# Performance work log

Measured on AMD Instinct MI355X. Metric: run time of the kernel, lower is better.

## Reference

```python
import jax, jax.numpy as jnp
import numpy as np

B, C, S = 16, 256, 1024
P_TOT, L = 24, 64
HEADS, DH = 8, 64
INNER = HEADS * DH
SPLITS = 8
SCALE = DH ** -0.5


def setup_inputs() -> dict:
    key = jax.random.key(0)
    k0, k1, k2, k3, k4 = jax.random.split(key, 5)
    w_scale = C ** -0.5  # Linear default-ish init scale, keeps softmax sane
    return {
        "x": jax.random.normal(k0, (B, C, S), jnp.float32),
        "prototypes": jax.random.normal(k1, (P_TOT, C, L), jnp.float32),
        "Wq": jax.random.normal(k2, (3, C, INNER), jnp.float32) * w_scale,
        "Wk": jax.random.normal(k3, (3, C, INNER), jnp.float32) * w_scale,
        "Wv": jax.random.normal(k4, (3, C, INNER), jnp.float32) * w_scale,
    }


def reference(x, prototypes, Wq, Wk, Wv):
    # x: [B, C, S] -> [B, S, C]; prototypes: [24, C, L]
    xp = jnp.transpose(x, (0, 2, 1))
    dists, idxs = [], []
    for i in range(3):  # fixed small loop over the 3 projection groups
        pg = prototypes[i * SPLITS:(i + 1) * SPLITS]          # [P, C, L]
        pp = jnp.transpose(pg, (0, 2, 1))                     # [P, L, C]
        # Q is identical across batch (the torch .repeat is a broadcast):
        q = (pp @ Wq[i]).reshape(SPLITS, L, HEADS, DH)        # [P, L, H, Dh]
        k = (xp @ Wk[i]).reshape(B, S, HEADS, DH)             # [B, S, H, Dh]
        v = (xp @ Wv[i]).reshape(B, S, HEADS, DH)
        dots = jnp.einsum('plhd,bshd->bhpls', q, k) * SCALE   # [B, H, P, L, S]
        attn = jax.nn.softmax(dots, axis=-1)
        out = jnp.einsum('bhpls,bshd->bhpld', attn, v)        # [B, H, P, L, Dh]
        out = jnp.transpose(out, (0, 2, 3, 1, 4)).reshape(B, SPLITS, L, INNER)
        q_full = q.reshape(SPLITS, L, INNER)[None]            # broadcast over B
        dist = jnp.mean((q_full - out) ** 2, axis=(2, 3))     # [B, P]
        heat = attn.mean(axis=(1, 3))                         # [B, P, S]
        dists.append(dist)
        idxs.append(jnp.argmax(heat, axis=-1))                # [B, P]
    return jnp.concatenate(dists, axis=1), jnp.concatenate(idxs, axis=1)
```

## Files before the change

kernel.cpp:

```cpp
#include <hip/hip_runtime.h>
#include <hip/hip_bf16.h>

#define Bq 16
#define Cc 256
#define Ss 1024
#define Ll 64
#define Hh 8
#define DHd 64
#define INN 512
#define Pp 8
#define KSC 0.18033688011111772f

#define QSLOT    262144
#define MDSLOT   131072
#define HEATSLOT 1048576
#define OUTSLOT  8388608
#define KSLOT    8388608
#define WSLOT    393216
#define HALFO    4194304

typedef short s16x8 __attribute__((ext_vector_type(8)));
typedef float f32x4 __attribute__((ext_vector_type(4)));
typedef unsigned u32x2 __attribute__((ext_vector_type(2)));
typedef unsigned u32x4 __attribute__((ext_vector_type(4)));

__device__ __forceinline__ unsigned short f2bf(float f) {
    unsigned u = __builtin_bit_cast(unsigned, f);
    u += 0x7FFF + ((u >> 16) & 1);
    return (unsigned short)(u >> 16);
}
__device__ __forceinline__ float bf2f(unsigned short h) {
    return __builtin_bit_cast(float, (unsigned)h << 16);
}
__device__ __forceinline__ unsigned cvt_pk_bf16(float a, float b) {
    unsigned r;
    asm volatile("v_cvt_pk_bf16_f32 %0, %1, %2" : "=v"(r) : "v"(a), "v"(b));
    return r;
}
__device__ __forceinline__ u32x2 ds_tr16(const unsigned short* p) {
    u32x2 d;
    asm volatile("ds_read_b64_tr_b16 %0, %1"
                 : "=v"(d)
                 : "v"((const __attribute__((address_space(3))) unsigned short*)p)
                 : "memory");
    return d;
}

__global__ __launch_bounds__(256) void wsplit_kernel(
        const float* __restrict__ Wk, const float* __restrict__ Wv,
        unsigned short* __restrict__ Wth, unsigned short* __restrict__ Wtl,
        unsigned short* __restrict__ Wvh) {
    __shared__ float tile[64][65];
    int blk = blockIdx.x;
    int i = blk >> 6, rem = blk & 63, mat = rem >> 5, ns = (rem >> 2) & 7, cb = rem & 3;
    int n0 = ns * 64, c0 = cb * 64, t = threadIdx.x;
    const float* W = (mat == 0 ? Wk : Wv) + (size_t)i * Cc * INN;
#pragma unroll
    for (int it = 0; it < 16; ++it) {
        int idx = t + it * 256; int cc = idx >> 6, nn = idx & 63;
        tile[cc][nn] = W[(size_t)(c0 + cc) * INN + n0 + nn];
    }
    __syncthreads();
#pragma unroll
    for (int it = 0; it < 16; ++it) {
        int idx = t + it * 256; int nn = idx >> 6, cc = idx & 63;
        float v = tile[cc][nn];
        unsigned short hi = f2bf(v);
        size_t o = (size_t)i * 131072 + (size_t)(n0 + nn) * Cc + c0 + cc;
        if (mat == 0) { Wth[o] = hi; Wtl[o] = f2bf(v - bf2f(hi)); }
        else          { Wvh[o] = hi; }
    }
}

__global__ __launch_bounds__(256) void qk_kernel(const float* __restrict__ prot,
                                                 const float* __restrict__ Wq,
                                                 float* __restrict__ qout) {
    __shared__ float pcol[4][256];
    int blk = blockIdx.x;
    int i = blk >> 7, rem = blk & 127, p = rem >> 4, l4 = rem & 15;
    int t = threadIdx.x;
    const float* W = Wq + (size_t)i * Cc * INN;
#pragma unroll
    for (int it = 0; it < 4; ++it) {
        int idx = t + it * 256; int ll = idx >> 8, cc = idx & 255;
        pcol[ll][cc] = prot[((size_t)(i * Pp + p) * Cc + cc) * Ll + l4 * 4 + ll];
    }
    __syncthreads();
    float a0[4] = {0, 0, 0, 0}, a1[4] = {0, 0, 0, 0};
#pragma unroll 4
    for (int c = 0; c < Cc; ++c) {
        float w0 = W[c * INN + t], w1 = W[c * INN + t + 256];
#pragma unroll
        for (int ll = 0; ll < 4; ++ll) {
            a0[ll] += pcol[ll][c] * w0;
            a1[ll] += pcol[ll][c] * w1;
        }
    }
#pragma unroll
    for (int ll = 0; ll < 4; ++ll) {
        float* qo = qout + (size_t)i * QSLOT + (size_t)(p * 64 + l4 * 4 + ll) * INN;
        qo[t] = a0[ll]; qo[t + 256] = a1[ll];
    }
}

__device__ __forceinline__ int xs_idx4(int s, int col4) {
    return s * 64 + (col4 ^ (s & 7));
}

__global__ __launch_bounds__(512, 2) void kv_kernel(
        const float* __restrict__ x, const unsigned short* __restrict__ WthA,
        const unsigned short* __restrict__ WtlA, const unsigned short* __restrict__ WvhA,
        unsigned short* __restrict__ Kh, unsigned short* __restrict__ Kl,
        unsigned short* __restrict__ Vt, int i0) {
    __shared__ unsigned xs[64 * 256];
    int bx = blockIdx.x & 255, i_local = blockIdx.x >> 8;
    int i = i0 + i_local;
    int b = bx >> 4, sb = bx & 15;
    int t = threadIdx.x, w = t >> 6, lane = t & 63, c = lane & 15, g = lane >> 4;
    int h = w;
    const unsigned short* wth = WthA + (size_t)i * 131072;
    const unsigned short* wtl = WtlA + (size_t)i * 131072;
    const unsigned short* wvh = WvhA + (size_t)i * 131072;
    unsigned short* Khp = Kh + (size_t)i_local * KSLOT;
    unsigned short* Klp = Kl + (size_t)i_local * KSLOT;
    unsigned short* Vtp = Vt + (size_t)i_local * KSLOT;

#pragma unroll
    for (int it = 0; it < 8; ++it) {
        int unit = t + it * 512;
        int ch = unit >> 4, sq = unit & 15;
        float4 v = *(const float4*)(x + ((size_t)b * Cc + ch) * Ss + sb * 64 + sq * 4);
        float vv[4] = {v.x, v.y, v.z, v.w};
#pragma unroll
        for (int e = 0; e < 4; ++e) {
            int s = sq * 4 + e;
            unsigned short hi = f2bf(vv[e]);
            unsigned short lo = f2bf(vv[e] - bf2f(hi));
            xs[s * 256 + ((ch >> 2) ^ (s & 7)) * 4 + (ch & 3)] =
                ((unsigned)hi << 16) | lo;
        }
    }
    __syncthreads();

    f32x4 accK[4][4], accV[4][4];
#pragma unroll
    for (int a = 0; a < 4; ++a)
#pragma unroll
      for (int s = 0; s < 4; ++s) {
        accK[a][s] = (f32x4){0.f, 0.f, 0.f, 0.f};
        accV[a][s] = (f32x4){0.f, 0.f, 0.f, 0.f};
      }

#pragma unroll
    for (int cs = 0; cs < 8; ++cs) {
        s16x8 xh[4], xl[4];
#pragma unroll
        for (int st = 0; st < 4; ++st) {
            int s = st * 16 + c;
            uint4 q0 = ((const uint4*)xs)[xs_idx4(s, cs * 8 + g * 2)];
            uint4 q1 = ((const uint4*)xs)[xs_idx4(s, cs * 8 + g * 2 + 1)];
            unsigned wrd[8] = {q0.x, q0.y, q0.z, q0.w, q1.x, q1.y, q1.z, q1.w};
            s16x8 fh, fl;
#pragma unroll
            for (int e = 0; e < 8; ++e) {
                fh[e] = (short)(wrd[e] >> 16);
                fl[e] = (short)(wrd[e] & 0xFFFF);
            }
            xh[st] = fh; xl[st] = fl;
        }
        int c0 = cs * 32 + g * 8;
#pragma unroll
        for (int nt = 0; nt < 4; ++nt) {
            int n = h * 64 + nt * 16 + c;
            s16x8 bh = __builtin_bit_cast(s16x8, *(const uint4*)(wth + (size_t)n * Cc + c0));
            s16x8 bl = __builtin_bit_cast(s16x8, *(const uint4*)(wtl + (size_t)n * Cc + c0));
            s16x8 bv = __builtin_bit_cast(s16x8, *(const uint4*)(wvh + (size_t)n * Cc + c0));
#pragma unroll
            for (int st = 0; st < 4; ++st) {
                accK[nt][st] = __builtin_amdgcn_mfma_f32_16x16x32_bf16(bh, xh[st], accK[nt][st], 0, 0, 0);
                accK[nt][st] = __builtin_amdgcn_mfma_f32_16x16x32_bf16(bh, xl[st], accK[nt][st], 0, 0, 0);
                accK[nt][st] = __builtin_amdgcn_mfma_f32_16x16x32_bf16(bl, xh[st], accK[nt][st], 0, 0, 0);
                accV[st][nt] = __builtin_amdgcn_mfma_f32_16x16x32_bf16(xh[st], bv, accV[st][nt], 0, 0, 0);
            }
        }
    }

#pragma unroll
    for (int nt = 0; nt < 4; ++nt)
#pragma unroll
      for (int st = 0; st < 4; ++st) {
        size_t kb = ((size_t)(b * Hh + h) * Ss + sb * 64 + st * 16 + c) * DHd
                    + nt * 16 + g * 4;
        unsigned short h0 = f2bf(accK[nt][st][0]), h1 = f2bf(accK[nt][st][1]);
        unsigned short h2 = f2bf(accK[nt][st][2]), h3 = f2bf(accK[nt][st][3]);
        uint2 ph; ph.x = h0 | ((unsigned)h1 << 16); ph.y = h2 | ((unsigned)h3 << 16);
        *(uint2*)(Khp + kb) = ph;
        unsigned short l0 = f2bf(accK[nt][st][0] - bf2f(h0));
        unsigned short l1 = f2bf(accK[nt][st][1] - bf2f(h1));
        unsigned short l2 = f2bf(accK[nt][st][2] - bf2f(h2));
        unsigned short l3 = f2bf(accK[nt][st][3] - bf2f(h3));
        uint2 pl; pl.x = l0 | ((unsigned)l1 << 16); pl.y = l2 | ((unsigned)l3 << 16);
        *(uint2*)(Klp + kb) = pl;
        size_t vb = ((size_t)(b * Hh + h) * DHd + nt * 16 + c) * Ss
                    + sb * 64 + st * 16 + g * 4;
        unsigned short v0 = f2bf(accV[st][nt][0]), v1 = f2bf(accV[st][nt][1]);
        unsigned short v2 = f2bf(accV[st][nt][2]), v3 = f2bf(accV[st][nt][3]);
        uint2 pv; pv.x = v0 | ((unsigned)v1 << 16); pv.y = v2 | ((unsigned)v3 << 16);
        *(uint2*)(Vtp + vb) = pv;
      }
}

__global__ __launch_bounds__(512, 2) void passA_kernel(
        const float* __restrict__ q, const unsigned short* __restrict__ Kh,
        float* __restrict__ md, int i0) {
    __shared__ unsigned short Klds[4096];
    int bx = blockIdx.x & 255, i_local = blockIdx.x >> 8;
    int i = i0 + i_local;
    int b = bx >> 4, h = (bx >> 1) & 7, sh = bx & 1;
    int t = threadIdx.x, p = t >> 6, lane = t & 63, c = lane & 15, g = lane >> 4;
    const float* qb = q + (size_t)i * QSLOT;
    const unsigned short* Khp = Kh + (size_t)i_local * KSLOT;

    s16x8 qh[4][2];
#pragma unroll
    for (int mt = 0; mt < 4; ++mt)
#pragma unroll
      for (int kt = 0; kt < 2; ++kt) {
        const float* qp = qb + (size_t)(p * 64 + mt * 16 + c) * INN + h * 64 + kt * 32 + g * 8;
        s16x8 f;
#pragma unroll
        for (int e = 0; e < 8; ++e) f[e] = (short)f2bf(qp[e] * KSC);
        qh[mt][kt] = f;
      }

    float d[4][4];
#pragma unroll
    for (int a = 0; a < 4; ++a)
#pragma unroll
      for (int r = 0; r < 4; ++r) d[a][r] = 0.f;

    int srow = t >> 3, g8 = t & 7, swz = g8 ^ (srow & 7);
    size_t rowb = (size_t)(b * Hh + h) * Ss;
    uint4 rK = *(const uint4*)(Khp + (rowb + sh * 512 + srow) * DHd + g8 * 8);

    for (int ch = 0; ch < 8; ++ch) {
        int sbase = sh * 512 + ch * 64;
        ((uint4*)Klds)[srow * 8 + swz] = rK;
        __syncthreads();
        if (ch < 7)
            rK = *(const uint4*)(Khp + (rowb + sbase + 64 + srow) * DHd + g8 * 8);

        f32x4 acc[4][4];
#pragma unroll
        for (int a = 0; a < 4; ++a)
#pragma unroll
          for (int s = 0; s < 4; ++s) acc[a][s] = (f32x4){0.f, 0.f, 0.f, 0.f};

#pragma unroll
        for (int kt = 0; kt < 2; ++kt)
#pragma unroll
          for (int st = 0; st < 4; ++st) {
            int srw = st * 16 + c;
            s16x8 kh = __builtin_bit_cast(s16x8,
                ((const uint4*)Klds)[srw * 8 + ((kt * 4 + g) ^ (srw & 7))]);
#pragma unroll
            for (int mt = 0; mt < 4; ++mt)
                acc[mt][st] = __builtin_amdgcn_mfma_f32_16x16x32_bf16(
                    qh[mt][kt], kh, acc[mt][st], 0, 0, 0);
          }

#pragma unroll
        for (int mt = 0; mt < 4; ++mt)
#pragma unroll
          for (int r = 0; r < 4; ++r)
            d[mt][r] += (__builtin_exp2f(acc[mt][0][r]) + __builtin_exp2f(acc[mt][1][r]))
                      + (__builtin_exp2f(acc[mt][2][r]) + __builtin_exp2f(acc[mt][3][r]));
        __syncthreads();
    }

    float* mdp = md + (size_t)i_local * MDSLOT;
#pragma unroll
    for (int mt = 0; mt < 4; ++mt)
#pragma unroll
      for (int r = 0; r < 4; ++r) {
        float v = d[mt][r];
        v += __shfl_xor(v, 1); v += __shfl_xor(v, 2);
        v += __shfl_xor(v, 4); v += __shfl_xor(v, 8);
        if (c == 0) {
            int row = mt * 16 + g * 4 + r;
            mdp[(((size_t)(b * Hh + h) * 2 + sh) * Pp + p) * Ll + row] = v;
        }
      }
}

__global__ __launch_bounds__(512) void passB_kernel(
        const float* __restrict__ q, const unsigned short* __restrict__ Kh,
        const unsigned short* __restrict__ Kl, const unsigned short* __restrict__ Vt,
        const float* __restrict__ md, float* __restrict__ heatp,
        unsigned short* __restrict__ outp, int i0) {
    __shared__ unsigned short Khl_[4096];
    __shared__ unsigned short Kll_[4096];
    __shared__ unsigned short Vtl_[4096];
    __shared__ unsigned short plds[8 * 2048];
    int bx = blockIdx.x & 255, i_local = blockIdx.x >> 8;
    int i = i0 + i_local;
    int b = bx >> 4, h = (bx >> 1) & 7, sh = bx & 1;
    int t = threadIdx.x, p = t >> 6, lane = t & 63, c = lane & 15, g = lane >> 4;
    const float* qb = q + (size_t)i * QSLOT;
    const unsigned short* Khp = Kh + (size_t)i_local * KSLOT;
    const unsigned short* Klp = Kl + (size_t)i_local * KSLOT;
    const unsigned short* Vtp = Vt + (size_t)i_local * KSLOT;
    const float* mdp = md + (size_t)i_local * MDSLOT;
    float* hpp = heatp + (size_t)i_local * HEATSLOT;
    unsigned short* opp = outp + (size_t)i_local * OUTSLOT;

    float rdf[4][4];
#pragma unroll
    for (int mt = 0; mt < 4; ++mt)
#pragma unroll
      for (int r = 0; r < 4; ++r) {
        int row = mt * 16 + g * 4 + r;
        size_t j0 = (((size_t)(b * Hh + h) * 2 + 0) * Pp + p) * Ll + row;
        size_t j1 = (((size_t)(b * Hh + h) * 2 + 1) * Pp + p) * Ll + row;
        rdf[mt][r] = 1.0f / (mdp[j0] + mdp[j1]);
      }

    s16x8 qh[4][2], ql[4][2];
#pragma unroll
    for (int mt = 0; mt < 4; ++mt)
#pragma unroll
      for (int kt = 0; kt < 2; ++kt) {
        const float* qp = qb + (size_t)(p * 64 + mt * 16 + c) * INN + h * 64 + kt * 32 + g * 8;
        s16x8 fh, fl;
#pragma unroll
        for (int e = 0; e < 8; ++e) {
            float v = qp[e] * KSC;
            unsigned short hi = f2bf(v);
            fh[e] = (short)hi;
            fl[e] = (short)f2bf(v - bf2f(hi));
        }
        qh[mt][kt] = fh; ql[mt][kt] = fl;
      }

    f32x4 o[4][4];
#pragma unroll
    for (int a = 0; a < 4; ++a)
#pragma unroll
      for (int s = 0; s < 4; ++s) o[a][s] = (f32x4){0.f, 0.f, 0.f, 0.f};

    int srow = t >> 3, g8 = t & 7, swz = g8 ^ (srow & 7);
    size_t rowK = (size_t)(b * Hh + h) * Ss;
    size_t rowV = ((size_t)(b * Hh + h) * DHd + srow) * Ss;
    uint4 rK = *(const uint4*)(Khp + (rowK + sh * 512 + srow) * DHd + g8 * 8);
    uint4 rL = *(const uint4*)(Klp + (rowK + sh * 512 + srow) * DHd + g8 * 8);
    uint4 rV = *(const uint4*)(Vtp + rowV + sh * 512 + g8 * 8);

    unsigned short* pwb = plds + p * 2048 + ((c >> 2) & 1) * 256 + (c & 3) * 16 + g * 4;
    const unsigned short* trb = plds + p * 2048 + g * 64 + c;

    for (int ch = 0; ch < 8; ++ch) {
        int sbase = sh * 512 + ch * 64;
        int dst = srow * 8 + swz;
        ((uint4*)Khl_)[dst] = rK;
        ((uint4*)Kll_)[dst] = rL;
        ((uint4*)Vtl_)[dst] = rV;
        __syncthreads();
        if (ch < 7) {
            rK = *(const uint4*)(Khp + (rowK + sbase + 64 + srow) * DHd + g8 * 8);
            rL = *(const uint4*)(Klp + (rowK + sbase + 64 + srow) * DHd + g8 * 8);
            rV = *(const uint4*)(Vtp + rowV + sbase + 64 + g8 * 8);
        }

#pragma unroll
        for (int half = 0; half < 2; ++half) {
            f32x4 sacc[4][2];
#pragma unroll
            for (int a = 0; a < 4; ++a)
#pragma unroll
              for (int s = 0; s < 2; ++s) sacc[a][s] = (f32x4){0.f, 0.f, 0.f, 0.f};

#pragma unroll
            for (int kt = 0; kt < 2; ++kt)
#pragma unroll
              for (int s2 = 0; s2 < 2; ++s2) {
                int srw = (half * 2 + s2) * 16 + c;
                int gi = srw * 8 + ((kt * 4 + g) ^ (srw & 7));
                s16x8 kh = __builtin_bit_cast(s16x8, ((const uint4*)Khl_)[gi]);
                s16x8 kl = __builtin_bit_cast(s16x8, ((const uint4*)Kll_)[gi]);
#pragma unroll
                for (int mt = 0; mt < 4; ++mt) {
                    sacc[mt][s2] = __builtin_amdgcn_mfma_f32_16x16x32_bf16(
                        qh[mt][kt], kh, sacc[mt][s2], 0, 0, 0);
                    sacc[mt][s2] = __builtin_amdgcn_mfma_f32_16x16x32_bf16(
                        qh[mt][kt], kl, sacc[mt][s2], 0, 0, 0);
                    sacc[mt][s2] = __builtin_amdgcn_mfma_f32_16x16x32_bf16(
                        ql[mt][kt], kh, sacc[mt][s2], 0, 0, 0);
                }
              }

#pragma unroll
            for (int s2 = 0; s2 < 2; ++s2) {
                float hs = 0.f;
#pragma unroll
                for (int mt = 0; mt < 4; ++mt) {
                    float pv0 = __builtin_exp2f(sacc[mt][s2][0]) * rdf[mt][0];
                    float pv1 = __builtin_exp2f(sacc[mt][s2][1]) * rdf[mt][1];
                    float pv2 = __builtin_exp2f(sacc[mt][s2][2]) * rdf[mt][2];
                    float pv3 = __builtin_exp2f(sacc[mt][s2][3]) * rdf[mt][3];
                    hs += (pv0 + pv1) + (pv2 + pv3);
                    uint2 pk;
                    pk.x = cvt_pk_bf16(pv0, pv1);
                    pk.y = cvt_pk_bf16(pv2, pv3);
                    *(uint2*)(pwb + mt * 512 + (s2 * 2 + (c >> 3)) * 64) = pk;
                }
                hs += __shfl_xor(hs, 16);
                hs += __shfl_xor(hs, 32);
                if (g == 0) {
                    int sgl = sbase + (half * 2 + s2) * 16 + c;
                    hpp[((size_t)(b * Pp + p) * Ss + sgl) * Hh + h] = hs;
                }
            }

            s16x8 vbf[4];
#pragma unroll
            for (int dht = 0; dht < 4; ++dht) {
                int row = dht * 16 + c;
                vbf[dht] = __builtin_bit_cast(s16x8,
                    ((const uint4*)Vtl_)[row * 8 + ((half * 4 + g) ^ (c & 7))]);
            }
            u32x2 ta[4][2];
#pragma unroll
            for (int mt = 0; mt < 4; ++mt) {
                ta[mt][0] = ds_tr16(trb + mt * 512);
                ta[mt][1] = ds_tr16(trb + mt * 512 + 256);
            }
            asm volatile("s_waitcnt lgkmcnt(0)" ::: "memory");
            __builtin_amdgcn_sched_barrier(0);
#pragma unroll
            for (int mt = 0; mt < 4; ++mt) {
                s16x8 pa = __builtin_bit_cast(s16x8,
                    (u32x4){ta[mt][0][0], ta[mt][0][1], ta[mt][1][0], ta[mt][1][1]});
#pragma unroll
                for (int dht = 0; dht < 4; ++dht)
                    o[mt][dht] = __builtin_amdgcn_mfma_f32_16x16x32_bf16(
                        pa, vbf[dht], o[mt][dht], 0, 0, 0);
            }
        }
        __syncthreads();
    }

#pragma unroll
    for (int mt = 0; mt < 4; ++mt)
#pragma unroll
      for (int dht = 0; dht < 4; ++dht)
#pragma unroll
        for (int r = 0; r < 4; ++r) {
            int row = mt * 16 + g * 4 + r;
            opp[(((((size_t)sh * Bq + b) * Hh + h) * Pp + p) * Ll + row) * DHd
                + dht * 16 + c] = f2bf(o[mt][dht][r]);
        }
}

__global__ __launch_bounds__(256) void fin_kernel(
        const float* __restrict__ heatp, const unsigned short* __restrict__ outp,
        const float* __restrict__ q, float* __restrict__ out, int i0) {
    __shared__ float rv[4];
    __shared__ int   ri[4];
    __shared__ float rs[4];
    int bx = blockIdx.x & 127, i_local = blockIdx.x >> 7;
    int i = i0 + i_local;
    int b = bx >> 3, p = bx & 7;
    int t = threadIdx.x, w = t >> 6, lane = t & 63;
    const float* qb = q + (size_t)i * QSLOT;
    const float* hp = heatp + (size_t)i_local * HEATSLOT;
    const unsigned short* ob = outp + (size_t)i_local * OUTSLOT;

    float best = -1e30f; int bidx = 0;
#pragma unroll
    for (int it = 0; it < 4; ++it) {
        int s = t + it * 256;
        const float* hv8 = hp + ((size_t)(b * Pp + p) * Ss + s) * Hh;
        float4 h0 = *(const float4*)hv8;
        float4 h1 = *(const float4*)(hv8 + 4);
        float hv = ((h0.x + h0.y) + (h0.z + h0.w)) + ((h1.x + h1.y) + (h1.z + h1.w));
        if (hv > best) { best = hv; bidx = s; }
    }
#pragma unroll
    for (int off = 1; off < 64; off <<= 1) {
        float vo = __shfl_xor(best, off);
        int   io = __shfl_xor(bidx, off);
        if (vo > best || (vo == best && io < bidx)) { best = vo; bidx = io; }
    }
    if (lane == 0) { rv[w] = best; ri[w] = bidx; }
    __syncthreads();
    if (t == 0) {
#pragma unroll
        for (int u = 1; u < 4; ++u)
            if (rv[u] > best || (rv[u] == best && ri[u] < bidx)) { best = rv[u]; bidx = ri[u]; }
        out[384 + b * 24 + i * Pp + p] = (float)bidx;
    }

    float sum = 0.f;
#pragma unroll 4
    for (int it = 0; it < 32; ++it) {
        int idx2 = t + it * 256;
        int dh4 = idx2 & 15, l = (idx2 >> 4) & 63, hh = idx2 >> 10;
        size_t base = ((size_t)((b * Hh + hh) * Pp + p) * 4096) + l * 64 + dh4 * 4;
        uint2 o0 = *(const uint2*)(ob + base);
        uint2 o1 = *(const uint2*)(ob + HALFO + base);
        float4 qv = *(const float4*)(qb + (size_t)(p * 64 + l) * INN + hh * 64 + dh4 * 4);
        float d0 = qv.x - (bf2f(o0.x & 0xFFFF) + bf2f(o1.x & 0xFFFF));
        float d1 = qv.y - (bf2f(o0.x >> 16)    + bf2f(o1.x >> 16));
        float d2 = qv.z - (bf2f(o0.y & 0xFFFF) + bf2f(o1.y & 0xFFFF));
        float d3 = qv.w - (bf2f(o0.y >> 16)    + bf2f(o1.y >> 16));
        sum += (d0 * d0 + d1 * d1) + (d2 * d2 + d3 * d3);
    }
#pragma unroll
    for (int off = 32; off; off >>= 1) sum += __shfl_down(sum, off);
    if (lane == 0) rs[w] = sum;
    __syncthreads();
    if (t == 0)
        out[b * 24 + i * Pp + p] = (rs[0] + rs[1] + rs[2] + rs[3]) / (float)(Ll * INN);
}

extern "C" void kernel_launch(void* const* d_in, const int* in_sizes, int n_in,
                              void* d_out, int out_size, void* d_ws, size_t ws_size,
                              hipStream_t stream) {
    const float* x    = (const float*)d_in[0];
    const float* prot = (const float*)d_in[1];
    const float* Wq   = (const float*)d_in[2];
    const float* Wk   = (const float*)d_in[3];
    const float* Wv   = (const float*)d_in[4];
    float* out = (float*)d_out;
    float* ws  = (float*)d_ws;

    const size_t needB = 220987392ull;
    bool batched = ws_size >= needB;
    size_t NS = batched ? 3 : 1;

    float* qbuf  = ws;
    float* md    = qbuf + 3 * QSLOT;
    float* heatp = md + NS * MDSLOT;
    unsigned short* outp = (unsigned short*)(heatp + NS * HEATSLOT);
    unsigned short* Kh  = outp + NS * OUTSLOT;
    unsigned short* Kl  = Kh + NS * KSLOT;
    unsigned short* Vt  = Kl + NS * KSLOT;
    unsigned short* Wth = Vt + NS * KSLOT;
    unsigned short* Wtl = Wth + 3 * WSLOT;
    unsigned short* Wvh = Wtl + 3 * WSLOT;

    wsplit_kernel<<<192, 256, 0, stream>>>(Wk, Wv, Wth, Wtl, Wvh);
    qk_kernel    <<<384, 256, 0, stream>>>(prot, Wq, qbuf);
    if (batched) {
        kv_kernel   <<<768, 512, 0, stream>>>(x, Wth, Wtl, Wvh, Kh, Kl, Vt, 0);
        passA_kernel<<<768, 512, 0, stream>>>(qbuf, Kh, md, 0);
        passB_kernel<<<768, 512, 0, stream>>>(qbuf, Kh, Kl, Vt, md, heatp, outp, 0);
        fin_kernel  <<<384, 256, 0, stream>>>(heatp, outp, qbuf, out, 0);
    } else {
        for (int i = 0; i < 3; ++i) {
            kv_kernel   <<<256, 512, 0, stream>>>(x, Wth, Wtl, Wvh, Kh, Kl, Vt, i);
            passA_kernel<<<256, 512, 0, stream>>>(qbuf, Kh, md, i);
            passB_kernel<<<256, 512, 0, stream>>>(qbuf, Kh, Kl, Vt, md, heatp, outp, i);
            fin_kernel  <<<128, 256, 0, stream>>>(heatp, outp, qbuf, out, i);
        }
    }
}
```

Before: 405.1 us.

## Switch split-bf16 compensated GEMMs to single fp16 MFMA passes

Replaces the hi/lo bf16 split (three MFMAs per product for K and scores) with a single fp16 MFMA per product. This drops the Kl buffer, Wtl weights and the ql/kl fragments, and halves the LDS footprint of x. It also folds the softmax normalizer into the score accumulator's initial value as -log2(denominator), removing a per-element multiply. This cuts MFMA work and memory traffic by roughly a factor of two to three in kv and passB, at the cost of fp16 range and precision risk on the scores, probabilities and outputs.

```diff
diff --git a/kernel.cpp b/kernel.cpp
--- a/kernel.cpp
+++ b/kernel.cpp
@@ -19,7 +19,8 @@
 #define WSLOT    393216
 #define HALFO    4194304
 
-typedef short s16x8 __attribute__((ext_vector_type(8)));
+typedef _Float16 f16x8 __attribute__((ext_vector_type(8)));
+typedef _Float16 f16x2 __attribute__((ext_vector_type(2)));
 typedef float f32x4 __attribute__((ext_vector_type(4)));
 typedef unsigned u32x2 __attribute__((ext_vector_type(2)));
 typedef unsigned u32x4 __attribute__((ext_vector_type(4)));
@@ -32,10 +33,9 @@
 __device__ __forceinline__ float bf2f(unsigned short h) {
     return __builtin_bit_cast(float, (unsigned)h << 16);
 }
-__device__ __forceinline__ unsigned cvt_pk_bf16(float a, float b) {
-    unsigned r;
-    asm volatile("v_cvt_pk_bf16_f32 %0, %1, %2" : "=v"(r) : "v"(a), "v"(b));
-    return r;
+__device__ __forceinline__ unsigned short f2h(float f) {
+    _Float16 h = (_Float16)f;
+    return __builtin_bit_cast(unsigned short, h);
 }
 __device__ __forceinline__ u32x2 ds_tr16(const unsigned short* p) {
     u32x2 d;
@@ -48,8 +48,7 @@
 
 __global__ __launch_bounds__(256) void wsplit_kernel(
         const float* __restrict__ Wk, const float* __restrict__ Wv,
-        unsigned short* __restrict__ Wth, unsigned short* __restrict__ Wtl,
-        unsigned short* __restrict__ Wvh) {
+        unsigned short* __restrict__ Wth, unsigned short* __restrict__ Wvh) {
     __shared__ float tile[64][65];
     int blk = blockIdx.x;
     int i = blk >> 6, rem = blk & 63, mat = rem >> 5, ns = (rem >> 2) & 7, cb = rem & 3;
@@ -65,10 +64,9 @@
     for (int it = 0; it < 16; ++it) {
         int idx = t + it * 256; int nn = idx >> 6, cc = idx & 63;
         float v = tile[cc][nn];
-        unsigned short hi = f2bf(v);
         size_t o = (size_t)i * 131072 + (size_t)(n0 + nn) * Cc + c0 + cc;
-        if (mat == 0) { Wth[o] = hi; Wtl[o] = f2bf(v - bf2f(hi)); }
-        else          { Wvh[o] = hi; }
+        if (mat == 0) Wth[o] = f2h(v);
+        else          Wvh[o] = f2h(v);
     }
 }
 
@@ -103,42 +101,32 @@
     }
 }
 
-__device__ __forceinline__ int xs_idx4(int s, int col4) {
-    return s * 64 + (col4 ^ (s & 7));
-}
-
 __global__ __launch_bounds__(512, 2) void kv_kernel(
         const float* __restrict__ x, const unsigned short* __restrict__ WthA,
-        const unsigned short* __restrict__ WtlA, const unsigned short* __restrict__ WvhA,
-        unsigned short* __restrict__ Kh, unsigned short* __restrict__ Kl,
-        unsigned short* __restrict__ Vt, int i0) {
-    __shared__ unsigned xs[64 * 256];
+        const unsigned short* __restrict__ WvhA,
+        unsigned short* __restrict__ Kh, unsigned short* __restrict__ Vt, int i0) {
+    __shared__ unsigned short xs[64 * 256];
     int bx = blockIdx.x & 255, i_local = blockIdx.x >> 8;
     int i = i0 + i_local;
     int b = bx >> 4, sb = bx & 15;
     int t = threadIdx.x, w = t >> 6, lane = t & 63, c = lane & 15, g = lane >> 4;
     int h = w;
     const unsigned short* wth = WthA + (size_t)i * 131072;
-    const unsigned short* wtl = WtlA + (size_t)i * 131072;
     const unsigned short* wvh = WvhA + (size_t)i * 131072;
     unsigned short* Khp = Kh + (size_t)i_local * KSLOT;
-    unsigned short* Klp = Kl + (size_t)i_local * KSLOT;
     unsigned short* Vtp = Vt + (size_t)i_local * KSLOT;
 
 #pragma unroll
     for (int it = 0; it < 8; ++it) {
         int unit = t + it * 512;
-        int ch = unit >> 4, sq = unit & 15;
-        float4 v = *(const float4*)(x + ((size_t)b * Cc + ch) * Ss + sb * 64 + sq * 4);
-        float vv[4] = {v.x, v.y, v.z, v.w};
-#pragma unroll
-        for (int e = 0; e < 4; ++e) {
-            int s = sq * 4 + e;
-            unsigned short hi = f2bf(vv[e]);
-            unsigned short lo = f2bf(vv[e] - bf2f(hi));
-            xs[s * 256 + ((ch >> 2) ^ (s & 7)) * 4 + (ch & 3)] =
-                ((unsigned)hi << 16) | lo;
-        }
+        int s = unit & 63, ch0 = (unit >> 6) * 4;
+        const float* xp = x + ((size_t)b * Cc + ch0) * Ss + sb * 64 + s;
+        float v0 = xp[0], v1 = xp[Ss], v2 = xp[2 * Ss], v3 = xp[3 * Ss];
+        uint2 pk;
+        pk.x = f2h(v0) | ((unsigned)f2h(v1) << 16);
+        pk.y = f2h(v2) | ((unsigned)f2h(v3) << 16);
+        int addr16 = s * 256 + (((ch0 >> 3) ^ (s & 7)) << 3) + (ch0 & 7);
+        *(uint2*)(xs + addr16) = pk;
     }
     __syncthreads();
 
@@ -153,34 +141,23 @@
 
 #pragma unroll
     for (int cs = 0; cs < 8; ++cs) {
-        s16x8 xh[4], xl[4];
+        f16x8 xf[4];
 #pragma unroll
         for (int st = 0; st < 4; ++st) {
             int s = st * 16 + c;
-            uint4 q0 = ((const uint4*)xs)[xs_idx4(s, cs * 8 + g * 2)];
-            uint4 q1 = ((const uint4*)xs)[xs_idx4(s, cs * 8 + g * 2 + 1)];
-            unsigned wrd[8] = {q0.x, q0.y, q0.z, q0.w, q1.x, q1.y, q1.z, q1.w};
-            s16x8 fh, fl;
-#pragma unroll
-            for (int e = 0; e < 8; ++e) {
-                fh[e] = (short)(wrd[e] >> 16);
-                fl[e] = (short)(wrd[e] & 0xFFFF);
-            }
-            xh[st] = fh; xl[st] = fl;
+            xf[st] = __builtin_bit_cast(f16x8,
+                ((const uint4*)xs)[s * 32 + ((cs * 4 + g) ^ (s & 7))]);
         }
         int c0 = cs * 32 + g * 8;
 #pragma unroll
         for (int nt = 0; nt < 4; ++nt) {
             int n = h * 64 + nt * 16 + c;
-            s16x8 bh = __builtin_bit_cast(s16x8, *(const uint4*)(wth + (size_t)n * Cc + c0));
-            s16x8 bl = __builtin_bit_cast(s16x8, *(const uint4*)(wtl + (size_t)n * Cc + c0));
-            s16x8 bv = __builtin_bit_cast(s16x8, *(const uint4*)(wvh + (size_t)n * Cc + c0));
+            f16x8 bk = __builtin_bit_cast(f16x8, *(const uint4*)(wth + (size_t)n * Cc + c0));
+            f16x8 bv = __builtin_bit_cast(f16x8, *(const uint4*)(wvh + (size_t)n * Cc + c0));
 #pragma unroll
             for (int st = 0; st < 4; ++st) {
-                accK[nt][st] = __builtin_amdgcn_mfma_f32_16x16x32_bf16(bh, xh[st], accK[nt][st], 0, 0, 0);
-                accK[nt][st] = __builtin_amdgcn_mfma_f32_16x16x32_bf16(bh, xl[st], accK[nt][st], 0, 0, 0);
-                accK[nt][st] = __builtin_amdgcn_mfma_f32_16x16x32_bf16(bl, xh[st], accK[nt][st], 0, 0, 0);
-                accV[st][nt] = __builtin_amdgcn_mfma_f32_16x16x32_bf16(xh[st], bv, accV[st][nt], 0, 0, 0);
+                accK[nt][st] = __builtin_amdgcn_mfma_f32_16x16x32_f16(bk, xf[st], accK[nt][st], 0, 0, 0);
+                accV[st][nt] = __builtin_amdgcn_mfma_f32_16x16x32_f16(xf[st], bv, accV[st][nt], 0, 0, 0);
             }
         }
     }
@@ -191,21 +168,15 @@
       for (int st = 0; st < 4; ++st) {
         size_t kb = ((size_t)(b * Hh + h) * Ss + sb * 64 + st * 16 + c) * DHd
                     + nt * 16 + g * 4;
-        unsigned short h0 = f2bf(accK[nt][st][0]), h1 = f2bf(accK[nt][st][1]);
-        unsigned short h2 = f2bf(accK[nt][st][2]), h3 = f2bf(accK[nt][st][3]);
-        uint2 ph; ph.x = h0 | ((unsigned)h1 << 16); ph.y = h2 | ((unsigned)h3 << 16);
+        uint2 ph;
+        ph.x = f2h(accK[nt][st][0]) | ((unsigned)f2h(accK[nt][st][1]) << 16);
+        ph.y = f2h(accK[nt][st][2]) | ((unsigned)f2h(accK[nt][st][3]) << 16);
         *(uint2*)(Khp + kb) = ph;
-        unsigned short l0 = f2bf(accK[nt][st][0] - bf2f(h0));
-        unsigned short l1 = f2bf(accK[nt][st][1] - bf2f(h1));
-        unsigned short l2 = f2bf(accK[nt][st][2] - bf2f(h2));
-        unsigned short l3 = f2bf(accK[nt][st][3] - bf2f(h3));
-        uint2 pl; pl.x = l0 | ((unsigned)l1 << 16); pl.y = l2 | ((unsigned)l3 << 16);
-        *(uint2*)(Klp + kb) = pl;
         size_t vb = ((size_t)(b * Hh + h) * DHd + nt * 16 + c) * Ss
                     + sb * 64 + st * 16 + g * 4;
-        unsigned short v0 = f2bf(accV[st][nt][0]), v1 = f2bf(accV[st][nt][1]);
-        unsigned short v2 = f2bf(accV[st][nt][2]), v3 = f2bf(accV[st][nt][3]);
-        uint2 pv; pv.x = v0 | ((unsigned)v1 << 16); pv.y = v2 | ((unsigned)v3 << 16);
+        uint2 pv;
+        pv.x = f2h(accV[st][nt][0]) | ((unsigned)f2h(accV[st][nt][1]) << 16);
+        pv.y = f2h(accV[st][nt][2]) | ((unsigned)f2h(accV[st][nt][3]) << 16);
         *(uint2*)(Vtp + vb) = pv;
       }
 }
@@ -221,16 +192,16 @@
     const float* qb = q + (size_t)i * QSLOT;
     const unsigned short* Khp = Kh + (size_t)i_local * KSLOT;
 
-    s16x8 qh[4][2];
+    f16x8 qf[4][2];
 #pragma unroll
     for (int mt = 0; mt < 4; ++mt)
 #pragma unroll
       for (int kt = 0; kt < 2; ++kt) {
         const float* qp = qb + (size_t)(p * 64 + mt * 16 + c) * INN + h * 64 + kt * 32 + g * 8;
-        s16x8 f;
-#pragma unroll
-        for (int e = 0; e < 8; ++e) f[e] = (short)f2bf(qp[e] * KSC);
-        qh[mt][kt] = f;
+        f16x8 f;
+#pragma unroll
+        for (int e = 0; e < 8; ++e) f[e] = (_Float16)(qp[e] * KSC);
+        qf[mt][kt] = f;
       }
 
     float d[4][4];
@@ -261,12 +232,12 @@
 #pragma unroll
           for (int st = 0; st < 4; ++st) {
             int srw = st * 16 + c;
-            s16x8 kh = __builtin_bit_cast(s16x8,
+            f16x8 kf = __builtin_bit_cast(f16x8,
                 ((const uint4*)Klds)[srw * 8 + ((kt * 4 + g) ^ (srw & 7))]);
 #pragma unroll
             for (int mt = 0; mt < 4; ++mt)
-                acc[mt][st] = __builtin_amdgcn_mfma_f32_16x16x32_bf16(
-                    qh[mt][kt], kh, acc[mt][st], 0, 0, 0);
+                acc[mt][st] = __builtin_amdgcn_mfma_f32_16x16x32_f16(
+                    qf[mt][kt], kf, acc[mt][st], 0, 0, 0);
           }
 
 #pragma unroll
@@ -295,11 +266,10 @@
 
 __global__ __launch_bounds__(512) void passB_kernel(
         const float* __restrict__ q, const unsigned short* __restrict__ Kh,
-        const unsigned short* __restrict__ Kl, const unsigned short* __restrict__ Vt,
+        const unsigned short* __restrict__ Vt,
         const float* __restrict__ md, float* __restrict__ heatp,
         unsigned short* __restrict__ outp, int i0) {
     __shared__ unsigned short Khl_[4096];
-    __shared__ unsigned short Kll_[4096];
     __shared__ unsigned short Vtl_[4096];
     __shared__ unsigned short plds[8 * 2048];
     int bx = blockIdx.x & 255, i_local = blockIdx.x >> 8;
@@ -308,13 +278,12 @@
     int t = threadIdx.x, p = t >> 6, lane = t & 63, c = lane & 15, g = lane >> 4;
     const float* qb = q + (size_t)i * QSLOT;
     const unsigned short* Khp = Kh + (size_t)i_local * KSLOT;
-    const unsigned short* Klp = Kl + (size_t)i_local * KSLOT;
     const unsigned short* Vtp = Vt + (size_t)i_local * KSLOT;
     const float* mdp = md + (size_t)i_local * MDSLOT;
     float* hpp = heatp + (size_t)i_local * HEATSLOT;
     unsigned short* opp = outp + (size_t)i_local * OUTSLOT;
 
-    float rdf[4][4];
+    f32x4 lgd[4];
 #pragma unroll
     for (int mt = 0; mt < 4; ++mt)
 #pragma unroll
@@ -322,24 +291,19 @@
         int row = mt * 16 + g * 4 + r;
         size_t j0 = (((size_t)(b * Hh + h) * 2 + 0) * Pp + p) * Ll + row;
         size_t j1 = (((size_t)(b * Hh + h) * 2 + 1) * Pp + p) * Ll + row;
-        rdf[mt][r] = 1.0f / (mdp[j0] + mdp[j1]);
+        lgd[mt][r] = -__builtin_log2f(mdp[j0] + mdp[j1]);
       }
 
-    s16x8 qh[4][2], ql[4][2];
+    f16x8 qf[4][2];
 #pragma unroll
     for (int mt = 0; mt < 4; ++mt)
 #pragma unroll
       for (int kt = 0; kt < 2; ++kt) {
         const float* qp = qb + (size_t)(p * 64 + mt * 16 + c) * INN + h * 64 + kt * 32 + g * 8;
-        s16x8 fh, fl;
-#pragma unroll
-        for (int e = 0; e < 8; ++e) {
-            float v = qp[e] * KSC;
-            unsigned short hi = f2bf(v);
-            fh[e] = (short)hi;
-            fl[e] = (short)f2bf(v - bf2f(hi));
-        }
-        qh[mt][kt] = fh; ql[mt][kt] = fl;
+        f16x8 f;
+#pragma unroll
+        for (int e = 0; e < 8; ++e) f[e] = (_Float16)(qp[e] * KSC);
+        qf[mt][kt] = f;
       }
 
     f32x4 o[4][4];
@@ -352,7 +316,6 @@
     size_t rowK = (size_t)(b * Hh + h) * Ss;
     size_t rowV = ((size_t)(b * Hh + h) * DHd + srow) * Ss;
     uint4 rK = *(const uint4*)(Khp + (rowK + sh * 512 + srow) * DHd + g8 * 8);
-    uint4 rL = *(const uint4*)(Klp + (rowK + sh * 512 + srow) * DHd + g8 * 8);
     uint4 rV = *(const uint4*)(Vtp + rowV + sh * 512 + g8 * 8);
 
     unsigned short* pwb = plds + p * 2048 + ((c >> 2) & 1) * 256 + (c & 3) * 16 + g * 4;
@@ -362,12 +325,10 @@
         int sbase = sh * 512 + ch * 64;
         int dst = srow * 8 + swz;
         ((uint4*)Khl_)[dst] = rK;
-        ((uint4*)Kll_)[dst] = rL;
         ((uint4*)Vtl_)[dst] = rV;
         __syncthreads();
         if (ch < 7) {
             rK = *(const uint4*)(Khp + (rowK + sbase + 64 + srow) * DHd + g8 * 8);
-            rL = *(const uint4*)(Klp + (rowK + sbase + 64 + srow) * DHd + g8 * 8);
             rV = *(const uint4*)(Vtp + rowV + sbase + 64 + g8 * 8);
         }
 
@@ -377,25 +338,19 @@
 #pragma unroll
             for (int a = 0; a < 4; ++a)
 #pragma unroll
-              for (int s = 0; s < 2; ++s) sacc[a][s] = (f32x4){0.f, 0.f, 0.f, 0.f};
+              for (int s = 0; s < 2; ++s) sacc[a][s] = lgd[a];
 
 #pragma unroll
             for (int kt = 0; kt < 2; ++kt)
 #pragma unroll
               for (int s2 = 0; s2 < 2; ++s2) {
                 int srw = (half * 2 + s2) * 16 + c;
-                int gi = srw * 8 + ((kt * 4 + g) ^ (srw & 7));
-                s16x8 kh = __builtin_bit_cast(s16x8, ((const uint4*)Khl_)[gi]);
-                s16x8 kl = __builtin_bit_cast(s16x8, ((const uint4*)Kll_)[gi]);
-#pragma unroll
-                for (int mt = 0; mt < 4; ++mt) {
-                    sacc[mt][s2] = __builtin_amdgcn_mfma_f32_16x16x32_bf16(
-                        qh[mt][kt], kh, sacc[mt][s2], 0, 0, 0);
-                    sacc[mt][s2] = __builtin_amdgcn_mfma_f32_16x16x32_bf16(
-                        qh[mt][kt], kl, sacc[mt][s2], 0, 0, 0);
-                    sacc[mt][s2] = __builtin_amdgcn_mfma_f32_16x16x32_bf16(
-                        ql[mt][kt], kh, sacc[mt][s2], 0, 0, 0);
-                }
+                f16x8 kf = __builtin_bit_cast(f16x8,
+                    ((const uint4*)Khl_)[srw * 8 + ((kt * 4 + g) ^ (srw & 7))]);
+#pragma unroll
+                for (int mt = 0; mt < 4; ++mt)
+                    sacc[mt][s2] = __builtin_amdgcn_mfma_f32_16x16x32_f16(
+                        qf[mt][kt], kf, sacc[mt][s2], 0, 0, 0);
               }
 
 #pragma unroll
@@ -403,14 +358,14 @@
                 float hs = 0.f;
 #pragma unroll
                 for (int mt = 0; mt < 4; ++mt) {
-                    float pv0 = __builtin_exp2f(sacc[mt][s2][0]) * rdf[mt][0];
-                    float pv1 = __builtin_exp2f(sacc[mt][s2][1]) * rdf[mt][1];
-                    float pv2 = __builtin_exp2f(sacc[mt][s2][2]) * rdf[mt][2];
-                    float pv3 = __builtin_exp2f(sacc[mt][s2][3]) * rdf[mt][3];
+                    float pv0 = __builtin_exp2f(sacc[mt][s2][0]);
+                    float pv1 = __builtin_exp2f(sacc[mt][s2][1]);
+                    float pv2 = __builtin_exp2f(sacc[mt][s2][2]);
+                    float pv3 = __builtin_exp2f(sacc[mt][s2][3]);
                     hs += (pv0 + pv1) + (pv2 + pv3);
                     uint2 pk;
-                    pk.x = cvt_pk_bf16(pv0, pv1);
-                    pk.y = cvt_pk_bf16(pv2, pv3);
+                    pk.x = __builtin_bit_cast(unsigned, __builtin_amdgcn_cvt_pkrtz(pv0, pv1));
+                    pk.y = __builtin_bit_cast(unsigned, __builtin_amdgcn_cvt_pkrtz(pv2, pv3));
                     *(uint2*)(pwb + mt * 512 + (s2 * 2 + (c >> 3)) * 64) = pk;
                 }
                 hs += __shfl_xor(hs, 16);
@@ -421,11 +376,11 @@
                 }
             }
 
-            s16x8 vbf[4];
+            f16x8 vbf[4];
 #pragma unroll
             for (int dht = 0; dht < 4; ++dht) {
                 int row = dht * 16 + c;
-                vbf[dht] = __builtin_bit_cast(s16x8,
+                vbf[dht] = __builtin_bit_cast(f16x8,
                     ((const uint4*)Vtl_)[row * 8 + ((half * 4 + g) ^ (c & 7))]);
             }
             u32x2 ta[4][2];
@@ -438,11 +393,11 @@
             __builtin_amdgcn_sched_barrier(0);
 #pragma unroll
             for (int mt = 0; mt < 4; ++mt) {
-                s16x8 pa = __builtin_bit_cast(s16x8,
+                f16x8 pa = __builtin_bit_cast(f16x8,
                     (u32x4){ta[mt][0][0], ta[mt][0][1], ta[mt][1][0], ta[mt][1][1]});
 #pragma unroll
                 for (int dht = 0; dht < 4; ++dht)
-                    o[mt][dht] = __builtin_amdgcn_mfma_f32_16x16x32_bf16(
+                    o[mt][dht] = __builtin_amdgcn_mfma_f32_16x16x32_f16(
                         pa, vbf[dht], o[mt][dht], 0, 0, 0);
             }
         }
@@ -534,7 +489,7 @@
     float* out = (float*)d_out;
     float* ws  = (float*)d_ws;
 
-    const size_t needB = 220987392ull;
+    const size_t needB = 173100000ull;
     bool batched = ws_size >= needB;
     size_t NS = batched ? 3 : 1;
 
@@ -543,24 +498,22 @@
     float* heatp = md + NS * MDSLOT;
     unsigned short* outp = (unsigned short*)(heatp + NS * HEATSLOT);
     unsigned short* Kh  = outp + NS * OUTSLOT;
-    unsigned short* Kl  = Kh + NS * KSLOT;
-    unsigned short* Vt  = Kl + NS * KSLOT;
+    unsigned short* Vt  = Kh + NS * KSLOT;
     unsigned short* Wth = Vt + NS * KSLOT;
-    unsigned short* Wtl = Wth + 3 * WSLOT;
-    unsigned short* Wvh = Wtl + 3 * WSLOT;
-
-    wsplit_kernel<<<192, 256, 0, stream>>>(Wk, Wv, Wth, Wtl, Wvh);
+    unsigned short* Wvh = Wth + 3 * WSLOT;
+
+    wsplit_kernel<<<192, 256, 0, stream>>>(Wk, Wv, Wth, Wvh);
     qk_kernel    <<<384, 256, 0, stream>>>(prot, Wq, qbuf);
     if (batched) {
-        kv_kernel   <<<768, 512, 0, stream>>>(x, Wth, Wtl, Wvh, Kh, Kl, Vt, 0);
+        kv_kernel   <<<768, 512, 0, stream>>>(x, Wth, Wvh, Kh, Vt, 0);
         passA_kernel<<<768, 512, 0, stream>>>(qbuf, Kh, md, 0);
-        passB_kernel<<<768, 512, 0, stream>>>(qbuf, Kh, Kl, Vt, md, heatp, outp, 0);
+        passB_kernel<<<768, 512, 0, stream>>>(qbuf, Kh, Vt, md, heatp, outp, 0);
         fin_kernel  <<<384, 256, 0, stream>>>(heatp, outp, qbuf, out, 0);
     } else {
         for (int i = 0; i < 3; ++i) {
-            kv_kernel   <<<256, 512, 0, stream>>>(x, Wth, Wtl, Wvh, Kh, Kl, Vt, i);
+            kv_kernel   <<<256, 512, 0, stream>>>(x, Wth, Wvh, Kh, Vt, i);
             passA_kernel<<<256, 512, 0, stream>>>(qbuf, Kh, md, i);
-            passB_kernel<<<256, 512, 0, stream>>>(qbuf, Kh, Kl, Vt, md, heatp, outp, i);
+            passB_kernel<<<256, 512, 0, stream>>>(qbuf, Kh, Vt, md, heatp, outp, i);
             fin_kernel  <<<128, 256, 0, stream>>>(heatp, outp, qbuf, out, i);
         }
     }
```

After: 356.0 us. 1.14x faster.
